# Kernel optimization log

Measured on AMD Instinct MI355X. Metric: run time of the kernel, lower is better.

Reference implementation:

```python
import jax, jax.numpy as jnp
import numpy as np

EPS = 1e-5
NEG_SLOPE = 0.2

def _conv1x1(x, w):
    # x: (B,C,N,K), w: (O,C) -> (B,O,N,K)
    return jnp.einsum('oc,bcnk->bonk', w, x)

def _bn(x, g, b, m, v):
    scale = g / jnp.sqrt(v + EPS)
    return x * scale[None, :, None, None] + (b - m * scale)[None, :, None, None]

def _lrelu(x):
    return jnp.where(x > 0, x, NEG_SLOPE * x)

def setup_inputs() -> dict:
    key = jax.random.key(0)
    specs = {
        'x': ((8, 6, 8192, 20), 'randn'),
        'trans_w': ((64, 6), 'randn'), 'trans_g': ((64,), 'rand'), 'trans_b': ((64,), 'randn'),
        'trans_m': ((64,), 'randn'), 'trans_v': ((64,), 'rand'),
        'pos_w1': ((64, 3), 'randn'), 'pos_g': ((64,), 'rand'), 'pos_b': ((64,), 'randn'),
        'pos_m': ((64,), 'randn'), 'pos_v': ((64,), 'rand'),
        'pos_w2': ((64, 64), 'randn'), 'pos_b2': ((64,), 'randn'),
        'gate_w1': ((16, 6), 'randn'), 'gate_g': ((16,), 'rand'), 'gate_b': ((16,), 'randn'),
        'gate_m': ((16,), 'randn'), 'gate_v': ((16,), 'rand'),
        'gate_w2': ((1, 16), 'randn'), 'gate_b2': ((1,), 'ones'),
        'attn_w1': ((16, 6), 'randn'), 'attn_g': ((16,), 'rand'), 'attn_b': ((16,), 'randn'),
        'attn_m': ((16,), 'randn'), 'attn_v': ((16,), 'rand'),
        'attn_w2': ((64, 16), 'randn'), 'attn_b2': ((64,), 'randn'),
    }
    out = {}
    for i, (name, (shape, fill)) in enumerate(specs.items()):
        k = jax.random.fold_in(key, i)
        if fill == 'randn':
            out[name] = jax.random.normal(k, shape, dtype=jnp.float32) * 0.1
        elif fill == 'rand':
            out[name] = jax.random.uniform(k, shape, dtype=jnp.float32)
        else:  # ones (gate bias init to 2.0 in original; scale ones)
            out[name] = jnp.ones(shape, dtype=jnp.float32) * 2.0
    return out

def reference(x, trans_w, trans_g, trans_b, trans_m, trans_v,
              pos_w1, pos_g, pos_b, pos_m, pos_v, pos_w2, pos_b2,
              gate_w1, gate_g, gate_b, gate_m, gate_v, gate_w2, gate_b2,
              attn_w1, attn_g, attn_b, attn_m, attn_v, attn_w2, attn_b2):
    in_channels = 3
    rel_pos = x[:, in_channels:in_channels + 3, :, :]  # (B,3,N,K)
    # pos_net: conv(3->C) + BN + LReLU + conv(C->C, bias)
    pos_h = _lrelu(_bn(_conv1x1(rel_pos, pos_w1), pos_g, pos_b, pos_m, pos_v))
    pos_enc = _conv1x1(pos_h, pos_w2) + pos_b2[None, :, None, None]
    # trans: conv(2*Cin->C) + BN + LReLU
    trans_feat = _lrelu(_bn(_conv1x1(x, trans_w), trans_g, trans_b, trans_m, trans_v)) + pos_enc
    # gate_net: conv(6->16)+BN+LReLU+conv(16->1,bias)+sigmoid (dropout=0 in eval)
    gate_h = _lrelu(_bn(_conv1x1(x, gate_w1), gate_g, gate_b, gate_m, gate_v))
    gate_map = jax.nn.sigmoid(_conv1x1(gate_h, gate_w2) + gate_b2[None, :, None, None])  # (B,1,N,K)
    clean_feat = trans_feat * gate_map
    # attn_net: conv(6->16)+BN+LReLU+conv(16->C,bias), then + pos_enc, softmax over K
    attn_h = _lrelu(_bn(_conv1x1(x, attn_w1), attn_g, attn_b, attn_m, attn_v))
    attn_logits = _conv1x1(attn_h, attn_w2) + attn_b2[None, :, None, None] + pos_enc
    attn_weights = jax.nn.softmax(attn_logits, axis=-1)
    out_attn = (trans_feat * attn_weights).sum(axis=-1)  # (B,C,N)
    out_max = clean_feat.max(axis=-1)                    # (B,C,N)
    return out_attn + out_max
```

## Files before the change

### kernel.cpp

```cpp
#include <hip/hip_runtime.h>
#include <math.h>

#define NEG 0.2f
#define EPSV 1e-5f

typedef _Float16 v8h __attribute__((ext_vector_type(8)));
typedef _Float16 v4h __attribute__((ext_vector_type(4)));
typedef _Float16 v2h __attribute__((ext_vector_type(2)));
typedef __fp16   f16x2 __attribute__((ext_vector_type(2)));
typedef float    v4f __attribute__((ext_vector_type(4)));

__device__ __forceinline__ float lrelu(float v) { return fmaxf(v, NEG * v); }

__device__ __forceinline__ v2h pk(float a, float b) {
    union { f16x2 i; v2h o; } u;
    u.i = __builtin_amdgcn_cvt_pkrtz(a, b);
    return u.o;
}

#define MFMA(a, b, c) __builtin_amdgcn_mfma_f32_16x16x32_f16((a), (b), (c), 0, 0, 0)

__global__ __launch_bounds__(256, 1)
void gsl_mfma(const float* __restrict__ x,
              const float* __restrict__ trans_w, const float* __restrict__ trans_g,
              const float* __restrict__ trans_b, const float* __restrict__ trans_m,
              const float* __restrict__ trans_v,
              const float* __restrict__ pos_w1, const float* __restrict__ pos_g,
              const float* __restrict__ pos_b, const float* __restrict__ pos_m,
              const float* __restrict__ pos_v, const float* __restrict__ pos_w2,
              const float* __restrict__ pos_b2,
              const float* __restrict__ gate_w1, const float* __restrict__ gate_g,
              const float* __restrict__ gate_b, const float* __restrict__ gate_m,
              const float* __restrict__ gate_v, const float* __restrict__ gate_w2,
              const float* __restrict__ gate_b2,
              const float* __restrict__ attn_w1, const float* __restrict__ attn_g,
              const float* __restrict__ attn_b, const float* __restrict__ attn_m,
              const float* __restrict__ attn_v, const float* __restrict__ attn_w2,
              const float* __restrict__ attn_b2,
              float* __restrict__ out)
{
    __shared__ _Float16 PHB[4][2][1152];
    __shared__ _Float16 AHB[4][2][448];

    const int tid  = threadIdx.x;
    const int wv   = tid >> 6;
    const int lane = tid & 63;
    const int p    = lane & 15;
    const int q    = lane >> 4;

    const int b = blockIdx.x >> 7;
    const int n = ((blockIdx.x & 127) << 6) | (wv << 4) | p;

    {
        _Float16* AH0 = &AHB[wv][0][0];
        const v4h zh = {(_Float16)0.f, (_Float16)0.f, (_Float16)0.f, (_Float16)0.f};
        for (int i = lane; i < 224; i += 64) *(v4h*)(AH0 + 4 * i) = zh;
    }

    v8h W2f[4][2], WTf[4], WP1f[4], WA2f[4], WA1f, WG1f;
    v4f pb2v[4];
    #pragma unroll
    for (int mt = 0; mt < 4; ++mt) {
        const int ch = mt * 16 + p;
        #pragma unroll
        for (int h = 0; h < 2; ++h)
            #pragma unroll
            for (int i = 0; i < 8; ++i)
                W2f[mt][h][i] = (_Float16)pos_w2[ch * 64 + h * 32 + q * 8 + i];
        #pragma unroll
        for (int i = 0; i < 8; ++i) {
            int k = q * 8 + i;
            WA2f[mt][i] = (k < 16) ? (_Float16)attn_w2[ch * 16 + k] : (_Float16)0.f;
        }
        {
            float st = trans_g[ch] * rsqrtf(trans_v[ch] + EPSV);
            float bt = trans_b[ch] - trans_m[ch] * st;
            #pragma unroll
            for (int i = 0; i < 8; ++i) {
                int k = q * 8 + i;
                float v = (k < 6) ? trans_w[ch * 6 + k] * st : ((k == 6) ? bt : 0.f);
                WTf[mt][i] = (_Float16)v;
            }
        }
        {
            float sp = pos_g[ch] * rsqrtf(pos_v[ch] + EPSV);
            float bp = pos_b[ch] - pos_m[ch] * sp;
            #pragma unroll
            for (int i = 0; i < 8; ++i) {
                int k = q * 8 + i;
                float v = (k >= 3 && k < 6) ? pos_w1[ch * 3 + (k - 3)] * sp
                                            : ((k == 6) ? bp : 0.f);
                WP1f[mt][i] = (_Float16)v;
            }
        }
        #pragma unroll
        for (int r = 0; r < 4; ++r)
            pb2v[mt][r] = pos_b2[mt * 16 + 4 * q + r];
    }
    {
        float sa = attn_g[p] * rsqrtf(attn_v[p] + EPSV);
        float ba = attn_b[p] - attn_m[p] * sa;
        #pragma unroll
        for (int i = 0; i < 8; ++i) {
            int k = q * 8 + i;
            float v = (k < 6) ? attn_w1[p * 6 + k] * sa : ((k == 6) ? ba : 0.f);
            WA1f[i] = (_Float16)v;
        }
    }
    {
        float sg = gate_g[p] * rsqrtf(gate_v[p] + EPSV);
        float bg = gate_b[p] - gate_m[p] * sg;
        #pragma unroll
        for (int i = 0; i < 8; ++i) {
            int k = q * 8 + i;
            float v = (k < 6) ? gate_w1[p * 6 + k] * sg : ((k == 6) ? bg : 0.f);
            WG1f[i] = (_Float16)v;
        }
    }
    float g2w[4];
    #pragma unroll
    for (int r = 0; r < 4; ++r) g2w[r] = gate_w2[4 * q + r];
    const float gb2v = gate_b2[0];

    _Float16* const PHbase = &PHB[wv][0][0];
    _Float16* const AHbase = &AHB[wv][0][0];

    const v4f zero = {0.f, 0.f, 0.f, 0.f};
    v4f den[4], num[4], cmx[4];
    #pragma unroll
    for (int mt = 0; mt < 4; ++mt) {
        den[mt] = zero; num[mt] = zero;
        cmx[mt] = (v4f){-3.4e38f, -3.4e38f, -3.4e38f, -3.4e38f};
    }

    const float* xb = x + ((size_t)(b * 6) * 8192 + n) * 20;

    float nx[6];
    #pragma unroll
    for (int c = 0; c < 6; ++c) nx[c] = xb[(size_t)c * 163840];

    v8h xv_cur;
    {
        union { v8h v; v2h h[4]; } u;
        u.h[0] = pk(nx[0], nx[1]);
        u.h[1] = pk(nx[2], nx[3]);
        u.h[2] = pk(nx[4], nx[5]);
        u.h[3] = (v2h){(_Float16)1.f, (_Float16)0.f};
        xv_cur = u.v;
    }
    #pragma unroll
    for (int c = 0; c < 6; ++c) nx[c] = xb[(size_t)c * 163840 + 1];

    {
        v4f php[4];
        #pragma unroll
        for (int mt = 0; mt < 4; ++mt) php[mt] = MFMA(WP1f[mt], xv_cur, zero);
        v4f ahp = MFMA(WA1f, xv_cur, zero);
        _Float16* PHW = PHbase + p * 72 + 4 * q;
        #pragma unroll
        for (int mt = 0; mt < 4; ++mt) {
            union { v4h v; v2h h[2]; } u;
            u.h[0] = pk(lrelu(php[mt][0]), lrelu(php[mt][1]));
            u.h[1] = pk(lrelu(php[mt][2]), lrelu(php[mt][3]));
            *(v4h*)(PHW + mt * 16) = u.v;
        }
        union { v4h v; v2h h[2]; } ua;
        ua.h[0] = pk(lrelu(ahp[0]), lrelu(ahp[1]));
        ua.h[1] = pk(lrelu(ahp[2]), lrelu(ahp[3]));
        *(v4h*)(AHbase + p * 24 + 4 * q) = ua.v;
    }

    #pragma unroll 1
    for (int k = 0; k < 20; ++k) {
        const int sel = k & 1;
        _Float16* PH = PHbase + sel * 1152;
        _Float16* AH = AHbase + sel * 448;
        v8h phf0 = *(const v8h*)(PH + p * 72 + 8 * q);
        v8h phf1 = *(const v8h*)(PH + p * 72 + 32 + 8 * q);
        v8h ahf  = *(const v8h*)(AH + p * 24 + 8 * q);

        v8h xv_nxt = xv_cur;
        if (k < 19) {
            union { v8h v; v2h h[4]; } u;
            u.h[0] = pk(nx[0], nx[1]);
            u.h[1] = pk(nx[2], nx[3]);
            u.h[2] = pk(nx[4], nx[5]);
            u.h[3] = (v2h){(_Float16)1.f, (_Float16)0.f};
            xv_nxt = u.v;
            const int kn = (k < 18) ? k + 2 : 19;
            #pragma unroll
            for (int c = 0; c < 6; ++c) nx[c] = xb[(size_t)c * 163840 + kn];

            v4f php[4];
            #pragma unroll
            for (int mt = 0; mt < 4; ++mt) php[mt] = MFMA(WP1f[mt], xv_nxt, zero);
            v4f ahp = MFMA(WA1f, xv_nxt, zero);
            _Float16* PHW = PHbase + (sel ^ 1) * 1152 + p * 72 + 4 * q;
            #pragma unroll
            for (int mt = 0; mt < 4; ++mt) {
                union { v4h v; v2h h[2]; } uu;
                uu.h[0] = pk(lrelu(php[mt][0]), lrelu(php[mt][1]));
                uu.h[1] = pk(lrelu(php[mt][2]), lrelu(php[mt][3]));
                *(v4h*)(PHW + mt * 16) = uu.v;
            }
            union { v4h v; v2h h[2]; } ua;
            ua.h[0] = pk(lrelu(ahp[0]), lrelu(ahp[1]));
            ua.h[1] = pk(lrelu(ahp[2]), lrelu(ahp[3]));
            *(v4h*)(AHbase + (sel ^ 1) * 448 + p * 24 + 4 * q) = ua.v;
        }

        v4f tfa[4];
        #pragma unroll
        for (int mt = 0; mt < 4; ++mt) tfa[mt] = MFMA(WTf[mt], xv_cur, zero);
        v4f ghp = MFMA(WG1f, xv_cur, zero);
        float ga = 0.f;
        #pragma unroll
        for (int r = 0; r < 4; ++r) ga += g2w[r] * lrelu(ghp[r]);
        ga += __shfl_xor(ga, 16);
        ga += __shfl_xor(ga, 32);
        const float gate = 1.f / (1.f + __expf(-(ga + gb2v)));

        v4f pe[4];
        #pragma unroll
        for (int mt = 0; mt < 4; ++mt) {
            pe[mt] = MFMA(W2f[mt][0], phf0, pb2v[mt]);
            pe[mt] = MFMA(W2f[mt][1], phf1, pe[mt]);
        }

        #pragma unroll
        for (int mt = 0; mt < 4; ++mt) {
            v4f tfv;
            #pragma unroll
            for (int r = 0; r < 4; ++r) tfv[r] = lrelu(tfa[mt][r]) + pe[mt][r];
            pe[mt] = MFMA(WA2f[mt], ahf, pe[mt]);
            #pragma unroll
            for (int r = 0; r < 4; ++r) {
                float e = __expf(pe[mt][r]);
                den[mt][r] += e;
                num[mt][r] += tfv[r] * e;
                cmx[mt][r] = fmaxf(cmx[mt][r], tfv[r] * gate);
            }
        }
        xv_cur = xv_nxt;
    }

    #pragma unroll
    for (int mt = 0; mt < 4; ++mt) {
        #pragma unroll
        for (int r = 0; r < 4; ++r) {
            const int ch = mt * 16 + 4 * q + r;
            out[((size_t)(b * 64 + ch)) * 8192 + n] =
                num[mt][r] / den[mt][r] + cmx[mt][r];
        }
    }
}

extern "C" void kernel_launch(void* const* d_in, const int* in_sizes, int n_in,
                              void* d_out, int out_size, void* d_ws, size_t ws_size,
                              hipStream_t stream) {
    const float* x       = (const float*)d_in[0];
    const float* trans_w = (const float*)d_in[1];
    const float* trans_g = (const float*)d_in[2];
    const float* trans_b = (const float*)d_in[3];
    const float* trans_m = (const float*)d_in[4];
    const float* trans_v = (const float*)d_in[5];
    const float* pos_w1  = (const float*)d_in[6];
    const float* pos_g   = (const float*)d_in[7];
    const float* pos_b   = (const float*)d_in[8];
    const float* pos_m   = (const float*)d_in[9];
    const float* pos_v   = (const float*)d_in[10];
    const float* pos_w2  = (const float*)d_in[11];
    const float* pos_b2  = (const float*)d_in[12];
    const float* gate_w1 = (const float*)d_in[13];
    const float* gate_g  = (const float*)d_in[14];
    const float* gate_b  = (const float*)d_in[15];
    const float* gate_m  = (const float*)d_in[16];
    const float* gate_v  = (const float*)d_in[17];
    const float* gate_w2 = (const float*)d_in[18];
    const float* gate_b2 = (const float*)d_in[19];
    const float* attn_w1 = (const float*)d_in[20];
    const float* attn_g  = (const float*)d_in[21];
    const float* attn_b  = (const float*)d_in[22];
    const float* attn_m  = (const float*)d_in[23];
    const float* attn_v  = (const float*)d_in[24];
    const float* attn_w2 = (const float*)d_in[25];
    const float* attn_b2 = (const float*)d_in[26];
    float* out = (float*)d_out;

    gsl_mfma<<<1024, 256, 0, stream>>>(
        x, trans_w, trans_g, trans_b, trans_m, trans_v,
        pos_w1, pos_g, pos_b, pos_m, pos_v, pos_w2, pos_b2,
        gate_w1, gate_g, gate_b, gate_m, gate_v, gate_w2, gate_b2,
        attn_w1, attn_g, attn_b, attn_m, attn_v, attn_w2, attn_b2,
        out);
}
```

Measured before the change: 206.6 us.

## Move rarely used MFMA weight fragments to shared memory and use packed-half lrelu

The pos_w1, attn_w1 and gate_w1 weight fragments, along with pos_b2, are now built once per block into shared memory and reloaded from LDS inside the loop instead of being held in registers. The aim is to lower register pressure, letting the compiler schedule better or avoid spills. The lrelu on hidden activations is now applied after packing to fp16 using packed-half max. The accumulation math is written as vector ops so packed fp32 instructions can be used. The trade-off is extra LDS reads every iteration plus a block-level barrier, and lrelu in fp16 rounds slightly differently.

```diff
diff --git a/kernel.cpp b/kernel.cpp
--- a/kernel.cpp
+++ b/kernel.cpp
@@ -11,6 +11,12 @@
 typedef float    v4f __attribute__((ext_vector_type(4)));
 
 __device__ __forceinline__ float lrelu(float v) { return fmaxf(v, NEG * v); }
+__device__ __forceinline__ v4f lrelu4(v4f v) {
+    return __builtin_elementwise_max(v, v * NEG);
+}
+__device__ __forceinline__ v2h lreluh2(v2h v) {
+    return __builtin_elementwise_max(v, v * (_Float16)NEG);
+}
 
 __device__ __forceinline__ v2h pk(float a, float b) {
     union { f16x2 i; v2h o; } u;
@@ -39,6 +45,8 @@
               const float* __restrict__ attn_b2,
               float* __restrict__ out)
 {
+    __shared__ _Float16 WH[3840];
+    __shared__ float    PB2[64];
     __shared__ _Float16 PHB[4][2][1152];
     __shared__ _Float16 AHB[4][2][448];
 
@@ -57,8 +65,36 @@
         for (int i = lane; i < 224; i += 64) *(v4h*)(AH0 + 4 * i) = zh;
     }
 
-    v8h W2f[4][2], WTf[4], WP1f[4], WA2f[4], WA1f, WG1f;
-    v4f pb2v[4];
+    if (tid < 64) {
+        const int c = tid;
+        float sp = pos_g[c] * rsqrtf(pos_v[c] + EPSV);
+        float bp = pos_b[c] - pos_m[c] * sp;
+        _Float16* row = WH + (c >> 4) * 640 + (c & 15) * 40;
+        for (int k = 0; k < 40; ++k) {
+            float v = (k >= 3 && k < 6) ? pos_w1[c * 3 + (k - 3)] * sp
+                                        : ((k == 6) ? bp : 0.f);
+            row[k] = (_Float16)v;
+        }
+        PB2[c] = pos_b2[c];
+    } else if (tid < 80) {
+        const int j = tid - 64;
+        float sa = attn_g[j] * rsqrtf(attn_v[j] + EPSV);
+        float ba = attn_b[j] - attn_m[j] * sa;
+        _Float16* row = WH + 2560 + j * 40;
+        for (int k = 0; k < 40; ++k)
+            row[k] = (_Float16)((k < 6) ? attn_w1[j * 6 + k] * sa
+                                        : ((k == 6) ? ba : 0.f));
+    } else if (tid < 96) {
+        const int j = tid - 80;
+        float sg = gate_g[j] * rsqrtf(gate_v[j] + EPSV);
+        float bg = gate_b[j] - gate_m[j] * sg;
+        _Float16* row = WH + 3200 + j * 40;
+        for (int k = 0; k < 40; ++k)
+            row[k] = (_Float16)((k < 6) ? gate_w1[j * 6 + k] * sg
+                                        : ((k == 6) ? bg : 0.f));
+    }
+
+    v8h W2f[4][2], WTf[4], WA2f[4];
     #pragma unroll
     for (int mt = 0; mt < 4; ++mt) {
         const int ch = mt * 16 + p;
@@ -72,55 +108,26 @@
             int k = q * 8 + i;
             WA2f[mt][i] = (k < 16) ? (_Float16)attn_w2[ch * 16 + k] : (_Float16)0.f;
         }
-        {
-            float st = trans_g[ch] * rsqrtf(trans_v[ch] + EPSV);
-            float bt = trans_b[ch] - trans_m[ch] * st;
-            #pragma unroll
-            for (int i = 0; i < 8; ++i) {
-                int k = q * 8 + i;
-                float v = (k < 6) ? trans_w[ch * 6 + k] * st : ((k == 6) ? bt : 0.f);
-                WTf[mt][i] = (_Float16)v;
-            }
-        }
-        {
-            float sp = pos_g[ch] * rsqrtf(pos_v[ch] + EPSV);
-            float bp = pos_b[ch] - pos_m[ch] * sp;
-            #pragma unroll
-            for (int i = 0; i < 8; ++i) {
-                int k = q * 8 + i;
-                float v = (k >= 3 && k < 6) ? pos_w1[ch * 3 + (k - 3)] * sp
-                                            : ((k == 6) ? bp : 0.f);
-                WP1f[mt][i] = (_Float16)v;
-            }
-        }
-        #pragma unroll
-        for (int r = 0; r < 4; ++r)
-            pb2v[mt][r] = pos_b2[mt * 16 + 4 * q + r];
-    }
-    {
-        float sa = attn_g[p] * rsqrtf(attn_v[p] + EPSV);
-        float ba = attn_b[p] - attn_m[p] * sa;
+        float st = trans_g[ch] * rsqrtf(trans_v[ch] + EPSV);
+        float bt = trans_b[ch] - trans_m[ch] * st;
         #pragma unroll
         for (int i = 0; i < 8; ++i) {
             int k = q * 8 + i;
-            float v = (k < 6) ? attn_w1[p * 6 + k] * sa : ((k == 6) ? ba : 0.f);
-            WA1f[i] = (_Float16)v;
-        }
-    }
-    {
-        float sg = gate_g[p] * rsqrtf(gate_v[p] + EPSV);
-        float bg = gate_b[p] - gate_m[p] * sg;
-        #pragma unroll
-        for (int i = 0; i < 8; ++i) {
-            int k = q * 8 + i;
-            float v = (k < 6) ? gate_w1[p * 6 + k] * sg : ((k == 6) ? bg : 0.f);
-            WG1f[i] = (_Float16)v;
+            float v = (k < 6) ? trans_w[ch * 6 + k] * st : ((k == 6) ? bt : 0.f);
+            WTf[mt][i] = (_Float16)v;
         }
     }
     float g2w[4];
     #pragma unroll
     for (int r = 0; r < 4; ++r) g2w[r] = gate_w2[4 * q + r];
     const float gb2v = gate_b2[0];
+
+    __syncthreads();
+
+    const _Float16* const WP1p = WH + p * 40 + q * 8;
+    const _Float16* const WA1p = WH + 2560 + p * 40 + q * 8;
+    const _Float16* const WG1p = WH + 3200 + p * 40 + q * 8;
+    const float* const    PB2p = PB2 + 4 * q;
 
     _Float16* const PHbase = &PHB[wv][0][0];
     _Float16* const AHbase = &AHB[wv][0][0];
@@ -154,19 +161,20 @@
     {
         v4f php[4];
         #pragma unroll
-        for (int mt = 0; mt < 4; ++mt) php[mt] = MFMA(WP1f[mt], xv_cur, zero);
-        v4f ahp = MFMA(WA1f, xv_cur, zero);
+        for (int mt = 0; mt < 4; ++mt)
+            php[mt] = MFMA(*(const v8h*)(WP1p + mt * 640), xv_cur, zero);
+        v4f ahp = MFMA(*(const v8h*)WA1p, xv_cur, zero);
         _Float16* PHW = PHbase + p * 72 + 4 * q;
         #pragma unroll
         for (int mt = 0; mt < 4; ++mt) {
             union { v4h v; v2h h[2]; } u;
-            u.h[0] = pk(lrelu(php[mt][0]), lrelu(php[mt][1]));
-            u.h[1] = pk(lrelu(php[mt][2]), lrelu(php[mt][3]));
+            u.h[0] = lreluh2(pk(php[mt][0], php[mt][1]));
+            u.h[1] = lreluh2(pk(php[mt][2], php[mt][3]));
             *(v4h*)(PHW + mt * 16) = u.v;
         }
         union { v4h v; v2h h[2]; } ua;
-        ua.h[0] = pk(lrelu(ahp[0]), lrelu(ahp[1]));
-        ua.h[1] = pk(lrelu(ahp[2]), lrelu(ahp[3]));
+        ua.h[0] = lreluh2(pk(ahp[0], ahp[1]));
+        ua.h[1] = lreluh2(pk(ahp[2], ahp[3]));
         *(v4h*)(AHbase + p * 24 + 4 * q) = ua.v;
     }
 
@@ -193,26 +201,27 @@
 
             v4f php[4];
             #pragma unroll
-            for (int mt = 0; mt < 4; ++mt) php[mt] = MFMA(WP1f[mt], xv_nxt, zero);
-            v4f ahp = MFMA(WA1f, xv_nxt, zero);
+            for (int mt = 0; mt < 4; ++mt)
+                php[mt] = MFMA(*(const v8h*)(WP1p + mt * 640), xv_nxt, zero);
+            v4f ahp = MFMA(*(const v8h*)WA1p, xv_nxt, zero);
             _Float16* PHW = PHbase + (sel ^ 1) * 1152 + p * 72 + 4 * q;
             #pragma unroll
             for (int mt = 0; mt < 4; ++mt) {
                 union { v4h v; v2h h[2]; } uu;
-                uu.h[0] = pk(lrelu(php[mt][0]), lrelu(php[mt][1]));
-                uu.h[1] = pk(lrelu(php[mt][2]), lrelu(php[mt][3]));
+                uu.h[0] = lreluh2(pk(php[mt][0], php[mt][1]));
+                uu.h[1] = lreluh2(pk(php[mt][2], php[mt][3]));
                 *(v4h*)(PHW + mt * 16) = uu.v;
             }
             union { v4h v; v2h h[2]; } ua;
-            ua.h[0] = pk(lrelu(ahp[0]), lrelu(ahp[1]));
-            ua.h[1] = pk(lrelu(ahp[2]), lrelu(ahp[3]));
+            ua.h[0] = lreluh2(pk(ahp[0], ahp[1]));
+            ua.h[1] = lreluh2(pk(ahp[2], ahp[3]));
             *(v4h*)(AHbase + (sel ^ 1) * 448 + p * 24 + 4 * q) = ua.v;
         }
 
         v4f tfa[4];
         #pragma unroll
         for (int mt = 0; mt < 4; ++mt) tfa[mt] = MFMA(WTf[mt], xv_cur, zero);
-        v4f ghp = MFMA(WG1f, xv_cur, zero);
+        v4f ghp = MFMA(*(const v8h*)WG1p, xv_cur, zero);
         float ga = 0.f;
         #pragma unroll
         for (int r = 0; r < 4; ++r) ga += g2w[r] * lrelu(ghp[r]);
@@ -223,23 +232,20 @@
         v4f pe[4];
         #pragma unroll
         for (int mt = 0; mt < 4; ++mt) {
-            pe[mt] = MFMA(W2f[mt][0], phf0, pb2v[mt]);
+            pe[mt] = MFMA(W2f[mt][0], phf0, *(const v4f*)(PB2p + mt * 16));
             pe[mt] = MFMA(W2f[mt][1], phf1, pe[mt]);
         }
 
         #pragma unroll
         for (int mt = 0; mt < 4; ++mt) {
-            v4f tfv;
-            #pragma unroll
-            for (int r = 0; r < 4; ++r) tfv[r] = lrelu(tfa[mt][r]) + pe[mt][r];
+            v4f tfv = lrelu4(tfa[mt]) + pe[mt];
             pe[mt] = MFMA(WA2f[mt], ahf, pe[mt]);
-            #pragma unroll
-            for (int r = 0; r < 4; ++r) {
-                float e = __expf(pe[mt][r]);
-                den[mt][r] += e;
-                num[mt][r] += tfv[r] * e;
-                cmx[mt][r] = fmaxf(cmx[mt][r], tfv[r] * gate);
-            }
+            v4f e;
+            #pragma unroll
+            for (int r = 0; r < 4; ++r) e[r] = __expf(pe[mt][r]);
+            den[mt] += e;
+            num[mt] += tfv * e;
+            cmx[mt] = __builtin_elementwise_max(cmx[mt], tfv * gate);
         }
         xv_cur = xv_nxt;
     }
```

New measurement: 197.9 us. 1.04x faster.
